# Kernel tuning notes

Hardware: AMD Instinct MI355X
Metric: run time of the kernel (lower is better)

Reference implementation:

```python
import jax, jax.numpy as jnp
import numpy as np

N_NODES = 100000
N_EDGES = 1600000
D_IN = 128
D_OUT = 128


def setup_inputs() -> dict:
    key = jax.random.key(0)
    k1, k2, k3, k4, k5 = jax.random.split(key, 5)
    features = jax.random.normal(k1, (N_NODES, D_IN), dtype=jnp.float32)
    weight = jax.random.normal(k2, (D_IN, D_OUT), dtype=jnp.float32)
    edge_val = jax.random.uniform(k3, (N_EDGES,), dtype=jnp.float32)
    edge_row = jax.random.randint(k4, (N_EDGES,), 0, N_NODES, dtype=jnp.int32)
    edge_col = jax.random.randint(k5, (N_EDGES,), 0, N_NODES, dtype=jnp.int32)
    return {"features": features, "weight": weight, "edge_val": edge_val,
            "edge_row": edge_row, "edge_col": edge_col}


def reference(features, weight, edge_val, edge_row, edge_col):
    # support = features @ W   (dense GEMM; torch.spmm with dense-strided lhs)
    support = features @ weight  # [N, D_OUT]
    # output = pre @ support   (sparse COO adjacency spmm)
    msgs = edge_val[:, None] * support[edge_col]  # [E, D_OUT] gather
    output = jax.ops.segment_sum(msgs, edge_row, num_segments=N_NODES)  # scatter-add
    # act == 'relu'; dropout p=0.0 is identity
    return jax.nn.relu(output)
```

## Files before the change

kernel.cpp:

```cpp
#include <hip/hip_runtime.h>
#include <hip/hip_bf16.h>


#define N_NODES 100000
#define N_EDGES 1600000
#define D 128
#define GEMM_BLOCKS ((N_NODES + 63) / 64)
#define CHUNK_A 8192
#define NBLK_A ((N_EDGES + CHUNK_A - 1) / CHUNK_A)
#define BUCKETS ((N_NODES + 127) / 128)
#define N_SCAN (BUCKETS * NBLK_A)
#define SCAN_BLK ((N_SCAN + 1023) / 1024)
#define BCAP 4608

typedef __attribute__((ext_vector_type(8))) short short8;
typedef __attribute__((ext_vector_type(4))) float floatx4;
typedef int  iv2 __attribute__((ext_vector_type(2)));
typedef int  iv4 __attribute__((ext_vector_type(4)));
typedef float fv4 __attribute__((ext_vector_type(4)));

union U16B { uint4 u4; short8 s8; uint u[4]; ushort us[8]; };

__device__ __forceinline__ ushort f32_to_bf16(float f) {
    uint b = __float_as_uint(f);
    return (ushort)((b + 0x7FFFu + ((b >> 16) & 1u)) >> 16);
}
__device__ __forceinline__ float bf16_to_f32(ushort u) {
    return __uint_as_float((uint)u << 16);
}

__device__ __forceinline__ void gemm_body(const float* __restrict__ feat,
                                          const float* __restrict__ W,
                                          ushort* __restrict__ support,
                                          ushort* __restrict__ Bp , int bid) {
    const int tid = threadIdx.x;
    const int wave = tid >> 6, lane = tid & 63;
    const int row0 = bid * 64 + wave * 16;
    const bool active = (row0 < N_NODES);
    const int m = lane & 15, g = lane >> 4;

    floatx4 acc[8];
    const floatx4 z = {0.f, 0.f, 0.f, 0.f};
    #pragma unroll
    for (int t = 0; t < 8; t++) acc[t] = z;

    const float* arow = feat + (size_t)(row0 + m) * D;
    #pragma unroll
    for (int h = 0; h < 2; h++) {
        if (h) __syncthreads();
        for (int e = tid; e < 64 * D; e += 256) {
            int kk = e >> 7, n = e & 127;
            Bp[(((kk >> 3) * D + n) << 3) | (kk & 7)] = f32_to_bf16(W[(h * 64 + kk) * D + n]);
        }
        __syncthreads();
        if (active) {
            #pragma unroll
            for (int ss = 0; ss < 2; ss++) {
                const int s = h * 2 + ss;
                float4 a0 = *(const float4*)(arow + s * 32 + g * 8);
                float4 a1 = *(const float4*)(arow + s * 32 + g * 8 + 4);
                U16B a;
                a.us[0] = f32_to_bf16(a0.x); a.us[1] = f32_to_bf16(a0.y);
                a.us[2] = f32_to_bf16(a0.z); a.us[3] = f32_to_bf16(a0.w);
                a.us[4] = f32_to_bf16(a1.x); a.us[5] = f32_to_bf16(a1.y);
                a.us[6] = f32_to_bf16(a1.z); a.us[7] = f32_to_bf16(a1.w);
                #pragma unroll
                for (int t = 0; t < 8; t++) {
                    const int chunk = (ss * 4 + g) * D + t * 16 + m;
                    U16B b; b.u4 = *(const uint4*)(Bp + chunk * 8);
                    acc[t] = __builtin_amdgcn_mfma_f32_16x16x32_bf16(a.s8, b.s8, acc[t], 0, 0, 0);
                }
            }
        }
    }
    if (active) {
        #pragma unroll
        for (int t = 0; t < 8; t++) {
            #pragma unroll
            for (int r = 0; r < 4; r++) {
                const int row = row0 + g * 4 + r;
                const int col = t * 16 + m;
                support[(size_t)row * D + col] = f32_to_bf16(acc[t][r]);
            }
        }
    }
}

__global__ __launch_bounds__(256) void gemm_kernel(const float* __restrict__ feat,
                                                   const float* __restrict__ W,
                                                   ushort* __restrict__ support,
                                                   const int* __restrict__ edge_row,
                                                   int* __restrict__ histT,
                                                   uint* __restrict__ st) {
    __shared__ ushort Bp[64 * D];
    __shared__ int hist[BUCKETS];
    const int bid = blockIdx.x, tid = threadIdx.x;
    const bool doHist = (histT != nullptr) && (bid < NBLK_A);
    if (doHist) {
        if (bid == 0 && tid < 256) st[tid] = 0u;
        for (int i = tid; i < BUCKETS; i += 256) hist[i] = 0;
    }
    gemm_body(feat, W, support, Bp, bid);
    if (doHist) {
        __syncthreads();
        const int base = bid * CHUNK_A;
        #pragma unroll
        for (int k = 0; k < CHUNK_A / 256; k++) {
            const int e = base + k * 256 + tid;
            if (e < N_EDGES) atomicAdd(&hist[edge_row[e] >> 7], 1);
        }
        __syncthreads();
        for (int i = tid; i < BUCKETS; i += 256) histT[i * NBLK_A + bid] = hist[i];
    }
}

__global__ __launch_bounds__(1024) void scan_kernel(const int* __restrict__ histT,
                                                    int* __restrict__ baseS,
                                                    int* __restrict__ bucketOff,
                                                    uint* __restrict__ st) {
    __shared__ int wsum[16];
    __shared__ int s_run, s_base;
    const int tid = threadIdx.x, b = blockIdx.x;
    const int gid = b * 1024 + tid;
    const int lane = tid & 63, wave = tid >> 6;

    const int v = (gid < N_SCAN) ? histT[gid] : 0;
    int x = v;
    #pragma unroll
    for (int d = 1; d < 64; d <<= 1) {
        int y = __shfl_up(x, d, 64);
        if (lane >= d) x += y;
    }
    if (lane == 63) wsum[wave] = x;
    __syncthreads();
    if (tid == 0) {
        int run = 0;
        #pragma unroll
        for (int w = 0; w < 16; w++) { int t = wsum[w]; wsum[w] = run; run += t; }
        s_run = run;
        __hip_atomic_store(&st[b], (1u << 30) | (uint)run,
                           __ATOMIC_RELEASE, __HIP_MEMORY_SCOPE_AGENT);
    }
    __syncthreads();
    if (wave == 0) {
        int P = 0;
        int base = b;
        bool done = (b == 0);
        while (!done) {
            const int j = base - 1 - lane;
            uint w;
            if (j >= 0) {
                do {
                    w = __hip_atomic_load(&st[j], __ATOMIC_ACQUIRE, __HIP_MEMORY_SCOPE_AGENT);
                } while ((w >> 30) == 0u);
            } else w = 2u << 30;
            const unsigned long long m2 = __ballot((w >> 30) == 2u);
            int contrib;
            if (m2) {
                const int fl = (int)__ffsll(m2) - 1;
                contrib = (lane <= fl) ? (int)(w & 0x3FFFFFFFu) : 0;
                done = true;
            } else {
                contrib = (int)(w & 0x3FFFFFFFu);
                base -= 64;
            }
            #pragma unroll
            for (int mm = 1; mm < 64; mm <<= 1) contrib += __shfl_xor(contrib, mm, 64);
            P += contrib;
        }
        if (lane == 0) {
            __hip_atomic_store(&st[b], (2u << 30) | (uint)(P + s_run),
                               __ATOMIC_RELEASE, __HIP_MEMORY_SCOPE_AGENT);
            s_base = P;
        }
    }
    __syncthreads();
    if (gid < N_SCAN) {
        const int excl = s_base + wsum[wave] + (x - v);
        baseS[gid] = excl;
        const int bucket = gid / NBLK_A;
        if (gid - bucket * NBLK_A == 0) bucketOff[bucket] = excl;
    }
    if (gid == 0) bucketOff[BUCKETS] = N_EDGES;
}

__global__ __launch_bounds__(256) void binscatter_kernel(const int* __restrict__ edge_row,
                                                         const int* __restrict__ edge_col,
                                                         const float* __restrict__ edge_val,
                                                         const int* __restrict__ baseS,
                                                         iv2* __restrict__ sorted) {
    __shared__ int cur[BUCKETS];
    const int tid = threadIdx.x, blk = blockIdx.x;
    for (int i = tid; i < BUCKETS; i += 256) cur[i] = baseS[i * NBLK_A + blk];
    __syncthreads();
    const int base = blk * CHUNK_A;
    #pragma unroll
    for (int k = 0; k < CHUNK_A / 256; k++) {
        const int e = base + k * 256 + tid;
        if (e < N_EDGES) {
            const int r = edge_row[e];
            const int p = atomicAdd(&cur[r >> 7], 1);
            iv2 pk;
            pk.x = ((r & 127) << 17) | edge_col[e];
            pk.y = __float_as_int(edge_val[e]);
            sorted[p] = pk;
        }
    }
}

__global__ __launch_bounds__(512) void bucket_accum_kernel(const int* __restrict__ bucketOff,
                                                           const iv2* __restrict__ sorted,
                                                           const ushort* __restrict__ support,
                                                           float* __restrict__ out) {
    __shared__ iv2 ebuf[BCAP];
    __shared__ ushort ord[BCAP];
    __shared__ int cnt[128], rowStart[128], cur[128];
    __shared__ int wtot;
    const int tid = threadIdx.x, b = blockIdx.x;
    const int s = bucketOff[b], eEnd = bucketOff[b + 1];
    const int nE = eEnd - s;

    if (tid < 128) cnt[tid] = 0;
    __syncthreads();
    for (int i = tid; i < nE; i += 512) {
        iv2 e = sorted[s + i];
        ebuf[i] = e;
        atomicAdd(&cnt[e.x >> 17], 1);
    }
    __syncthreads();
    const int lane = tid & 63;
    const int myc = (tid < 128) ? cnt[tid] : 0;
    int x = myc;
    #pragma unroll
    for (int d = 1; d < 64; d <<= 1) {
        int y = __shfl_up(x, d, 64);
        if (lane >= d) x += y;
    }
    if (tid == 63) wtot = x;
    __syncthreads();
    if (tid < 128) {
        const int excl = x - myc + ((tid >= 64) ? wtot : 0);
        rowStart[tid] = excl;
        cur[tid] = excl;
    }
    __syncthreads();
    for (int i = tid; i < nE; i += 512) {
        const int rl = ebuf[i].x >> 17;
        const int p = atomicAdd(&cur[rl], 1);
        ord[p] = (ushort)i;
    }
    __syncthreads();

    const int g = tid >> 4, part = tid & 15;
    #pragma unroll
    for (int t = 0; t < 4; t++) {
        const int rl = g * 4 + t;
        const int grow = (b << 7) + rl;
        if (grow >= N_NODES) break;
        const int rs = rowStart[rl], re = rs + cnt[rl];

        float acc0[8], acc1[8];
        #pragma unroll
        for (int i = 0; i < 8; i++) { acc0[i] = 0.f; acc1[i] = 0.f; }

        int k = rs;
        for (; k + 3 < re; k += 4) {
            const int i0 = ord[k], i1 = ord[k + 1], i2 = ord[k + 2], i3 = ord[k + 3];
            const iv2 e0 = ebuf[i0], e1 = ebuf[i1], e2 = ebuf[i2], e3 = ebuf[i3];
            U16B s0; s0.u4 = *(const uint4*)(support + (size_t)(e0.x & 0x1FFFF) * D + part * 8);
            U16B s1; s1.u4 = *(const uint4*)(support + (size_t)(e1.x & 0x1FFFF) * D + part * 8);
            U16B s2; s2.u4 = *(const uint4*)(support + (size_t)(e2.x & 0x1FFFF) * D + part * 8);
            U16B s3; s3.u4 = *(const uint4*)(support + (size_t)(e3.x & 0x1FFFF) * D + part * 8);
            const float v0 = __int_as_float(e0.y);
            const float v1 = __int_as_float(e1.y);
            const float v2 = __int_as_float(e2.y);
            const float v3 = __int_as_float(e3.y);
            #pragma unroll
            for (int i = 0; i < 8; i++) {
                acc0[i] += bf16_to_f32(s0.us[i]) * v0;
                acc1[i] += bf16_to_f32(s1.us[i]) * v1;
                acc0[i] += bf16_to_f32(s2.us[i]) * v2;
                acc1[i] += bf16_to_f32(s3.us[i]) * v3;
            }
        }
        for (; k < re; ++k) {
            const int i0 = ord[k];
            const iv2 e0 = ebuf[i0];
            U16B s0; s0.u4 = *(const uint4*)(support + (size_t)(e0.x & 0x1FFFF) * D + part * 8);
            const float v0 = __int_as_float(e0.y);
            #pragma unroll
            for (int i = 0; i < 8; i++) acc0[i] += bf16_to_f32(s0.us[i]) * v0;
        }

        fv4 lo, hi;
        lo.x = fmaxf(acc0[0] + acc1[0], 0.f); lo.y = fmaxf(acc0[1] + acc1[1], 0.f);
        lo.z = fmaxf(acc0[2] + acc1[2], 0.f); lo.w = fmaxf(acc0[3] + acc1[3], 0.f);
        hi.x = fmaxf(acc0[4] + acc1[4], 0.f); hi.y = fmaxf(acc0[5] + acc1[5], 0.f);
        hi.z = fmaxf(acc0[6] + acc1[6], 0.f); hi.w = fmaxf(acc0[7] + acc1[7], 0.f);
        float* dst = out + (size_t)grow * D + part * 8;
        __builtin_nontemporal_store(lo, (fv4*)dst);
        __builtin_nontemporal_store(hi, (fv4*)(dst + 4));
    }
}

__global__ __launch_bounds__(256) void zero_f4_kernel(float4* __restrict__ acc, int n4) {
    int i = blockIdx.x * 256 + threadIdx.x;
    if (i < n4) acc[i] = make_float4(0.f, 0.f, 0.f, 0.f);
}
__global__ __launch_bounds__(256) void spmm_kernel(const ushort* __restrict__ support,
                                                   const float* __restrict__ edge_val,
                                                   const int* __restrict__ edge_row,
                                                   const int* __restrict__ edge_col,
                                                   float* __restrict__ out) {
    const long gtid = (long)blockIdx.x * 256 + threadIdx.x;
    const int edge = (int)(gtid >> 4);
    const int part = (int)(gtid & 15);
    if (edge >= N_EDGES) return;
    const int col = edge_col[edge];
    const int row = edge_row[edge];
    const float v = edge_val[edge];
    U16B s; s.u4 = *(const uint4*)(support + (size_t)col * D + part * 8);
    float* dst = out + (size_t)row * D + part * 8;
    #pragma unroll
    for (int i = 0; i < 8; i++) unsafeAtomicAdd(dst + i, bf16_to_f32(s.us[i]) * v);
}
__global__ __launch_bounds__(256) void relu_kernel(float4* __restrict__ out, int n4) {
    int i = blockIdx.x * 256 + threadIdx.x;
    if (i >= n4) return;
    float4 a = out[i];
    a.x = fmaxf(a.x, 0.f); a.y = fmaxf(a.y, 0.f);
    a.z = fmaxf(a.z, 0.f); a.w = fmaxf(a.w, 0.f);
    out[i] = a;
}

extern "C" void kernel_launch(void* const* d_in, const int* in_sizes, int n_in,
                              void* d_out, int out_size, void* d_ws, size_t ws_size,
                              hipStream_t stream) {
    (void)in_sizes; (void)n_in; (void)out_size;
    const float* feat     = (const float*)d_in[0];
    const float* W        = (const float*)d_in[1];
    const float* edge_val = (const float*)d_in[2];
    const int*   edge_row = (const int*)d_in[3];
    const int*   edge_col = (const int*)d_in[4];
    float* out = (float*)d_out;

    char* ws = (char*)d_ws;
    size_t o = 0;
    ushort* support  = (ushort*)(ws + o); o += (size_t)N_NODES * D * sizeof(ushort);
    int*    histT    = (int*)(ws + o);    o += ((size_t)N_SCAN * 4 + 15) & ~15ull;
    int*    baseS    = (int*)(ws + o);    o += ((size_t)N_SCAN * 4 + 15) & ~15ull;
    int*    bucketOff= (int*)(ws + o);    o += ((size_t)(BUCKETS + 1) * 4 + 15) & ~15ull;
    uint*   st       = (uint*)(ws + o);   o += 256 * 4;
    iv2*    sorted   = (iv2*)(ws + o);    o += (size_t)N_EDGES * 8;
    const size_t needed = o;

    if (ws_size >= needed) {
        gemm_kernel<<<GEMM_BLOCKS, 256, 0, stream>>>(feat, W, support, edge_row, histT, st);
        scan_kernel<<<SCAN_BLK, 1024, 0, stream>>>(histT, baseS, bucketOff, st);
        binscatter_kernel<<<NBLK_A, 256, 0, stream>>>(edge_row, edge_col, edge_val,
                                                      baseS, sorted);
        bucket_accum_kernel<<<BUCKETS, 512, 0, stream>>>(bucketOff, sorted, support, out);
    } else {
        const int n4 = N_NODES * D / 4;
        zero_f4_kernel<<<(n4 + 255) / 256, 256, 0, stream>>>((float4*)out, n4);
        gemm_kernel<<<GEMM_BLOCKS, 256, 0, stream>>>(feat, W, support, nullptr, nullptr, nullptr);
        spmm_kernel<<<(int)(((long)N_EDGES * 16 + 255) / 256), 256, 0, stream>>>(
            support, edge_val, edge_row, edge_col, out);
        relu_kernel<<<(n4 + 255) / 256, 256, 0, stream>>>((float4*)out, n4);
    }
}
```

Baseline: 264.2 us.

## Pre-convert W to bf16 once, drop LDS staging in GEMM and bucket accum

Adds a small kernel that converts W to bf16 in MFMA-friendly order once. The GEMM blocks then read B fragments straight from global/L2 instead of each block converting and staging W in LDS with barriers. It also transposes the scan output so binscatter reads its bucket offsets contiguously. The bucket-accumulate kernel no longer copies edges into LDS and rereads them from global memory, which cuts LDS use and may raise occupancy, at the cost of extra global/L2 traffic. In the fallback path, WB is used even when the workspace may be too small, which risks an out-of-bounds write.

```diff
diff --git a/kernel.cpp b/kernel.cpp
--- a/kernel.cpp
+++ b/kernel.cpp
@@ -29,70 +29,21 @@
     return __uint_as_float((uint)u << 16);
 }
 
-__device__ __forceinline__ void gemm_body(const float* __restrict__ feat,
-                                          const float* __restrict__ W,
-                                          ushort* __restrict__ support,
-                                          ushort* __restrict__ Bp , int bid) {
-    const int tid = threadIdx.x;
-    const int wave = tid >> 6, lane = tid & 63;
-    const int row0 = bid * 64 + wave * 16;
-    const bool active = (row0 < N_NODES);
-    const int m = lane & 15, g = lane >> 4;
-
-    floatx4 acc[8];
-    const floatx4 z = {0.f, 0.f, 0.f, 0.f};
-    #pragma unroll
-    for (int t = 0; t < 8; t++) acc[t] = z;
-
-    const float* arow = feat + (size_t)(row0 + m) * D;
-    #pragma unroll
-    for (int h = 0; h < 2; h++) {
-        if (h) __syncthreads();
-        for (int e = tid; e < 64 * D; e += 256) {
-            int kk = e >> 7, n = e & 127;
-            Bp[(((kk >> 3) * D + n) << 3) | (kk & 7)] = f32_to_bf16(W[(h * 64 + kk) * D + n]);
-        }
-        __syncthreads();
-        if (active) {
-            #pragma unroll
-            for (int ss = 0; ss < 2; ss++) {
-                const int s = h * 2 + ss;
-                float4 a0 = *(const float4*)(arow + s * 32 + g * 8);
-                float4 a1 = *(const float4*)(arow + s * 32 + g * 8 + 4);
-                U16B a;
-                a.us[0] = f32_to_bf16(a0.x); a.us[1] = f32_to_bf16(a0.y);
-                a.us[2] = f32_to_bf16(a0.z); a.us[3] = f32_to_bf16(a0.w);
-                a.us[4] = f32_to_bf16(a1.x); a.us[5] = f32_to_bf16(a1.y);
-                a.us[6] = f32_to_bf16(a1.z); a.us[7] = f32_to_bf16(a1.w);
-                #pragma unroll
-                for (int t = 0; t < 8; t++) {
-                    const int chunk = (ss * 4 + g) * D + t * 16 + m;
-                    U16B b; b.u4 = *(const uint4*)(Bp + chunk * 8);
-                    acc[t] = __builtin_amdgcn_mfma_f32_16x16x32_bf16(a.s8, b.s8, acc[t], 0, 0, 0);
-                }
-            }
-        }
-    }
-    if (active) {
-        #pragma unroll
-        for (int t = 0; t < 8; t++) {
-            #pragma unroll
-            for (int r = 0; r < 4; r++) {
-                const int row = row0 + g * 4 + r;
-                const int col = t * 16 + m;
-                support[(size_t)row * D + col] = f32_to_bf16(acc[t][r]);
-            }
-        }
+__global__ __launch_bounds__(256) void wconv_kernel(const float* __restrict__ W,
+                                                    ushort* __restrict__ WB) {
+    const int o = blockIdx.x * 256 + threadIdx.x;
+    if (o < D * D) {
+        const int K8 = o >> 10, rem = o & 1023, n = rem >> 3, j = rem & 7;
+        WB[o] = f32_to_bf16(W[(K8 * 8 + j) * D + n]);
     }
 }
 
 __global__ __launch_bounds__(256) void gemm_kernel(const float* __restrict__ feat,
-                                                   const float* __restrict__ W,
+                                                   const ushort* __restrict__ WB,
                                                    ushort* __restrict__ support,
                                                    const int* __restrict__ edge_row,
                                                    int* __restrict__ histT,
                                                    uint* __restrict__ st) {
-    __shared__ ushort Bp[64 * D];
     __shared__ int hist[BUCKETS];
     const int bid = blockIdx.x, tid = threadIdx.x;
     const bool doHist = (histT != nullptr) && (bid < NBLK_A);
@@ -100,7 +51,45 @@
         if (bid == 0 && tid < 256) st[tid] = 0u;
         for (int i = tid; i < BUCKETS; i += 256) hist[i] = 0;
     }
-    gemm_body(feat, W, support, Bp, bid);
+
+    const int wave = tid >> 6, lane = tid & 63;
+    const int row0 = bid * 64 + wave * 16;
+    const int m = lane & 15, g = lane >> 4;
+
+    if (row0 < N_NODES) {
+        floatx4 acc[8];
+        const floatx4 z = {0.f, 0.f, 0.f, 0.f};
+        #pragma unroll
+        for (int t = 0; t < 8; t++) acc[t] = z;
+
+        const float* arow = feat + (size_t)(row0 + m) * D;
+        const ushort* wb = WB + g * 1024 + m * 8;
+        #pragma unroll
+        for (int s = 0; s < 4; s++) {
+            float4 a0 = *(const float4*)(arow + s * 32 + g * 8);
+            float4 a1 = *(const float4*)(arow + s * 32 + g * 8 + 4);
+            U16B a;
+            a.us[0] = f32_to_bf16(a0.x); a.us[1] = f32_to_bf16(a0.y);
+            a.us[2] = f32_to_bf16(a0.z); a.us[3] = f32_to_bf16(a0.w);
+            a.us[4] = f32_to_bf16(a1.x); a.us[5] = f32_to_bf16(a1.y);
+            a.us[6] = f32_to_bf16(a1.z); a.us[7] = f32_to_bf16(a1.w);
+            #pragma unroll
+            for (int t = 0; t < 8; t++) {
+                U16B b; b.u4 = *(const uint4*)(wb + s * 4096 + t * 128);
+                acc[t] = __builtin_amdgcn_mfma_f32_16x16x32_bf16(a.s8, b.s8, acc[t], 0, 0, 0);
+            }
+        }
+        #pragma unroll
+        for (int t = 0; t < 8; t++) {
+            #pragma unroll
+            for (int r = 0; r < 4; r++) {
+                const int row = row0 + g * 4 + r;
+                const int col = t * 16 + m;
+                support[(size_t)row * D + col] = f32_to_bf16(acc[t][r]);
+            }
+        }
+    }
+
     if (doHist) {
         __syncthreads();
         const int base = bid * CHUNK_A;
@@ -115,7 +104,7 @@
 }
 
 __global__ __launch_bounds__(1024) void scan_kernel(const int* __restrict__ histT,
-                                                    int* __restrict__ baseS,
+                                                    int* __restrict__ baseST,
                                                     int* __restrict__ bucketOff,
                                                     uint* __restrict__ st) {
     __shared__ int wsum[16];
@@ -177,9 +166,10 @@
     __syncthreads();
     if (gid < N_SCAN) {
         const int excl = s_base + wsum[wave] + (x - v);
-        baseS[gid] = excl;
         const int bucket = gid / NBLK_A;
-        if (gid - bucket * NBLK_A == 0) bucketOff[bucket] = excl;
+        const int blk = gid - bucket * NBLK_A;
+        baseST[blk * BUCKETS + bucket] = excl;
+        if (blk == 0) bucketOff[bucket] = excl;
     }
     if (gid == 0) bucketOff[BUCKETS] = N_EDGES;
 }
@@ -187,11 +177,11 @@
 __global__ __launch_bounds__(256) void binscatter_kernel(const int* __restrict__ edge_row,
                                                          const int* __restrict__ edge_col,
                                                          const float* __restrict__ edge_val,
-                                                         const int* __restrict__ baseS,
+                                                         const int* __restrict__ baseST,
                                                          iv2* __restrict__ sorted) {
     __shared__ int cur[BUCKETS];
     const int tid = threadIdx.x, blk = blockIdx.x;
-    for (int i = tid; i < BUCKETS; i += 256) cur[i] = baseS[i * NBLK_A + blk];
+    for (int i = tid; i < BUCKETS; i += 256) cur[i] = baseST[blk * BUCKETS + i];
     __syncthreads();
     const int base = blk * CHUNK_A;
     #pragma unroll
@@ -212,7 +202,6 @@
                                                            const iv2* __restrict__ sorted,
                                                            const ushort* __restrict__ support,
                                                            float* __restrict__ out) {
-    __shared__ iv2 ebuf[BCAP];
     __shared__ ushort ord[BCAP];
     __shared__ int cnt[128], rowStart[128], cur[128];
     __shared__ int wtot;
@@ -222,11 +211,8 @@
 
     if (tid < 128) cnt[tid] = 0;
     __syncthreads();
-    for (int i = tid; i < nE; i += 512) {
-        iv2 e = sorted[s + i];
-        ebuf[i] = e;
-        atomicAdd(&cnt[e.x >> 17], 1);
-    }
+    for (int i = tid; i < nE; i += 512)
+        atomicAdd(&cnt[sorted[s + i].x >> 17], 1);
     __syncthreads();
     const int lane = tid & 63;
     const int myc = (tid < 128) ? cnt[tid] : 0;
@@ -245,7 +231,7 @@
     }
     __syncthreads();
     for (int i = tid; i < nE; i += 512) {
-        const int rl = ebuf[i].x >> 17;
+        const int rl = sorted[s + i].x >> 17;
         const int p = atomicAdd(&cur[rl], 1);
         ord[p] = (ushort)i;
     }
@@ -266,7 +252,8 @@
         int k = rs;
         for (; k + 3 < re; k += 4) {
             const int i0 = ord[k], i1 = ord[k + 1], i2 = ord[k + 2], i3 = ord[k + 3];
-            const iv2 e0 = ebuf[i0], e1 = ebuf[i1], e2 = ebuf[i2], e3 = ebuf[i3];
+            const iv2 e0 = sorted[s + i0], e1 = sorted[s + i1];
+            const iv2 e2 = sorted[s + i2], e3 = sorted[s + i3];
             U16B s0; s0.u4 = *(const uint4*)(support + (size_t)(e0.x & 0x1FFFF) * D + part * 8);
             U16B s1; s1.u4 = *(const uint4*)(support + (size_t)(e1.x & 0x1FFFF) * D + part * 8);
             U16B s2; s2.u4 = *(const uint4*)(support + (size_t)(e2.x & 0x1FFFF) * D + part * 8);
@@ -285,7 +272,7 @@
         }
         for (; k < re; ++k) {
             const int i0 = ord[k];
-            const iv2 e0 = ebuf[i0];
+            const iv2 e0 = sorted[s + i0];
             U16B s0; s0.u4 = *(const uint4*)(support + (size_t)(e0.x & 0x1FFFF) * D + part * 8);
             const float v0 = __int_as_float(e0.y);
             #pragma unroll
@@ -347,23 +334,27 @@
     char* ws = (char*)d_ws;
     size_t o = 0;
     ushort* support  = (ushort*)(ws + o); o += (size_t)N_NODES * D * sizeof(ushort);
+    ushort* WB       = (ushort*)(ws + o); o += (size_t)D * D * sizeof(ushort);
     int*    histT    = (int*)(ws + o);    o += ((size_t)N_SCAN * 4 + 15) & ~15ull;
-    int*    baseS    = (int*)(ws + o);    o += ((size_t)N_SCAN * 4 + 15) & ~15ull;
+    int*    baseST   = (int*)(ws + o);    o += ((size_t)N_SCAN * 4 + 15) & ~15ull;
     int*    bucketOff= (int*)(ws + o);    o += ((size_t)(BUCKETS + 1) * 4 + 15) & ~15ull;
     uint*   st       = (uint*)(ws + o);   o += 256 * 4;
     iv2*    sorted   = (iv2*)(ws + o);    o += (size_t)N_EDGES * 8;
     const size_t needed = o;
 
     if (ws_size >= needed) {
-        gemm_kernel<<<GEMM_BLOCKS, 256, 0, stream>>>(feat, W, support, edge_row, histT, st);
-        scan_kernel<<<SCAN_BLK, 1024, 0, stream>>>(histT, baseS, bucketOff, st);
+        wconv_kernel<<<(D * D + 255) / 256, 256, 0, stream>>>(W, WB);
+        gemm_kernel<<<GEMM_BLOCKS, 256, 0, stream>>>(feat, WB, support, edge_row, histT, st);
+        scan_kernel<<<SCAN_BLK, 1024, 0, stream>>>(histT, baseST, bucketOff, st);
         binscatter_kernel<<<NBLK_A, 256, 0, stream>>>(edge_row, edge_col, edge_val,
-                                                      baseS, sorted);
+                                                      baseST, sorted);
         bucket_accum_kernel<<<BUCKETS, 512, 0, stream>>>(bucketOff, sorted, support, out);
     } else {
         const int n4 = N_NODES * D / 4;
         zero_f4_kernel<<<(n4 + 255) / 256, 256, 0, stream>>>((float4*)out, n4);
-        gemm_kernel<<<GEMM_BLOCKS, 256, 0, stream>>>(feat, W, support, nullptr, nullptr, nullptr);
+        wconv_kernel<<<(D * D + 255) / 256, 256, 0, stream>>>(W, WB);
+        gemm_kernel<<<GEMM_BLOCKS, 256, 0, stream>>>(feat, WB, support, nullptr, nullptr,
+                                                     nullptr);
         spmm_kernel<<<(int)(((long)N_EDGES * 16 + 255) / 256), 256, 0, stream>>>(
             support, edge_val, edge_row, edge_col, out);
         relu_kernel<<<(n4 + 255) / 256, 256, 0, stream>>>((float4*)out, n4);
```

After: 274.9 us. 4.0% more time.
